# Kernel tuning notes

Hardware: AMD Instinct MI355X
Metric: run time of the kernel (lower is better)

## Reference

```python
import jax, jax.numpy as jnp
import numpy as np

B, S, TK, H, E, V, OOV = 16, 8, 400, 256, 128, 50000, 50
H2 = 2 * H


def setup_inputs() -> dict:
    key = jax.random.key(0)
    ks = jax.random.split(key, 24)
    std = 0.02
    d = {}
    d["y_t_1"] = jax.random.randint(ks[0], (B,), 0, V)
    d["h0"] = jax.random.normal(ks[1], (B, H), jnp.float32)
    d["c0"] = jax.random.normal(ks[2], (B, H), jnp.float32)
    d["encoder_output"] = jax.random.normal(ks[3], (B, S, TK, H2), jnp.float32)
    d["section_output"] = jax.random.normal(ks[4], (B, S, H2), jnp.float32)
    d["enc_padding_mask"] = jnp.ones((B, S, TK), jnp.float32)
    d["c_t_1"] = jax.random.normal(ks[5], (B, H2), jnp.float32)
    d["extra_zeros"] = jnp.zeros((B, OOV), jnp.float32)
    d["enc_batch_extend_vocab"] = jax.random.randint(ks[6], (B, S * TK), 0, V + OOV)
    d["coverage"] = jnp.zeros((B, S, TK), jnp.float32)
    d["gamma"] = jnp.ones((B, S, TK), jnp.float32)
    # learned parameters
    d["embedding"] = std * jax.random.normal(ks[7], (V, E), jnp.float32)
    d["W_xc"] = std * jax.random.normal(ks[8], (H2 + E, E), jnp.float32)
    d["b_xc"] = jnp.zeros((E,), jnp.float32)
    d["W_ih"] = std * jax.random.normal(ks[9], (E, 4 * H), jnp.float32)
    d["b_ih"] = jnp.zeros((4 * H,), jnp.float32)
    d["W_hh"] = std * jax.random.normal(ks[10], (H, 4 * H), jnp.float32)
    # pytorch init sets forget-gate bias (2nd quarter) to 1
    d["b_hh"] = jnp.zeros((4 * H,), jnp.float32).at[H:2 * H].set(1.0)
    d["Wh_sec"] = std * jax.random.normal(ks[11], (H2, H2), jnp.float32)
    d["Wd_sec"] = std * jax.random.normal(ks[12], (H2, H2), jnp.float32)
    d["bd_sec"] = jnp.zeros((H2,), jnp.float32)
    d["v_sec"] = std * jax.random.normal(ks[13], (H2, 1), jnp.float32)
    d["Wh_w"] = std * jax.random.normal(ks[14], (H2, H2), jnp.float32)
    d["Wc_w"] = std * jax.random.normal(ks[15], (H2,), jnp.float32)
    d["Wd_w"] = std * jax.random.normal(ks[16], (H2, H2), jnp.float32)
    d["bd_w"] = jnp.zeros((H2,), jnp.float32)
    d["v_w"] = std * jax.random.normal(ks[17], (H2, 1), jnp.float32)
    d["W_pgen"] = std * jax.random.normal(ks[18], (4 * H + E, 1), jnp.float32)
    d["b_pgen"] = jnp.zeros((1,), jnp.float32)
    d["W_out1"] = std * jax.random.normal(ks[19], (3 * H, H), jnp.float32)
    d["b_out1"] = jnp.zeros((H,), jnp.float32)
    d["W_out2"] = std * jax.random.normal(ks[20], (H, V), jnp.float32)
    d["b_out2"] = jnp.zeros((V,), jnp.float32)
    return d


def reference(y_t_1, h0, c0, encoder_output, section_output, enc_padding_mask,
              c_t_1, extra_zeros, enc_batch_extend_vocab, coverage, gamma,
              embedding, W_xc, b_xc, W_ih, b_ih, W_hh, b_hh,
              Wh_sec, Wd_sec, bd_sec, v_sec,
              Wh_w, Wc_w, Wd_w, bd_w, v_w,
              W_pgen, b_pgen, W_out1, b_out1, W_out2, b_out2):
    # embedding + input context projection
    emb = embedding[y_t_1]                                      # [B,E]
    x = jnp.concatenate([c_t_1, emb], axis=1) @ W_xc + b_xc     # [B,E]
    # single-step LSTM (pytorch gate order i,f,g,o)
    gates = x @ W_ih + b_ih + h0 @ W_hh + b_hh                  # [B,4H]
    i, f, g, o = jnp.split(gates, 4, axis=1)
    c = jax.nn.sigmoid(f) * c0 + jax.nn.sigmoid(i) * jnp.tanh(g)
    h = jax.nn.sigmoid(o) * jnp.tanh(c)
    s_t_hat = jnp.concatenate([h, c], axis=1)                   # [B,2H]
    # section attention -> beta [B,S]
    e_sec = jnp.tanh(section_output @ Wh_sec + (s_t_hat @ Wd_sec + bd_sec)[:, None, :])
    sc_sec = jnp.squeeze(e_sec @ v_sec, -1)                     # [B,S]
    beta = jax.nn.softmax(sc_sec, axis=1)
    beta = beta / beta.sum(axis=1, keepdims=True)
    # word attention with coverage feature
    att = encoder_output @ Wh_w + (s_t_hat @ Wd_w + bd_w)[:, None, None, :]
    att = att + coverage[..., None] * Wc_w                      # [B,S,TK,2H]
    sc_w = jnp.squeeze(jnp.tanh(att) @ v_w, -1)                 # [B,S,TK]
    ws = (beta[:, :, None] * sc_w).reshape(B, S * TK)
    mask = enc_padding_mask.reshape(B, S * TK)
    ad = jax.nn.softmax(ws, axis=1) * mask
    attn = ad / ad.sum(axis=1, keepdims=True)                   # [B,S*TK]
    c_t = jnp.einsum('bt,btn->bn', attn, encoder_output.reshape(B, S * TK, H2))
    cov = coverage + attn.reshape(B, S, TK)
    # pointer-gen gate
    p_gen = jax.nn.sigmoid(jnp.concatenate([c_t, s_t_hat, x], axis=1) @ W_pgen + b_pgen)  # [B,1]
    # output vocab distribution
    out = jnp.concatenate([h, c_t], axis=1) @ W_out1 + b_out1
    vocab_dist = jax.nn.softmax(out @ W_out2 + b_out2, axis=1)  # [B,V]
    vd = jnp.concatenate([p_gen * vocab_dist, extra_zeros], axis=1)  # [B,V+OOV]
    ad_ = (1.0 - p_gen) * attn
    rows = jnp.arange(B)[:, None]
    final_dist = vd.at[rows, enc_batch_extend_vocab].add(ad_)
    return (final_dist, h, c, c_t, attn, p_gen, cov)
```

## Files before the change

kernel.cpp:

```cpp
#include <hip/hip_runtime.h>
#include <math.h>

#define BB   16
#define SS   8
#define TKK  400
#define HH   256
#define EE   128
#define VV   50000
#define OOVV 50
#define HH2  512
#define STK  (SS*TKK)
#define VOO  (VV+OOVV)

#define OFF_X     0
#define OFF_ST    2048
#define OFF_SD    10240
#define OFF_WD    18432
#define OFF_SCSEC 26752
#define OFF_SCW   26880
#define OFF_CT    78080
#define OFF_OUT1  86272
#define OFF_PGEN  90368
#define OFF_PSUM  93520
#define OFF_BT    113040

#define O_FD   0
#define O_H    800800
#define O_C    804896
#define O_CT   808992
#define O_ATTN 817184
#define O_PGEN 868384
#define O_COV  868400

#define NLB 391
#define GEMM_NB 800

typedef __attribute__((ext_vector_type(8))) short bf16x8;
typedef __attribute__((ext_vector_type(4))) float f32x4;

__device__ __forceinline__ float sigm(float x){ return 1.0f/(1.0f+expf(-x)); }

__device__ __forceinline__ unsigned short f2b(float f){
  unsigned int u = __float_as_uint(f);
  unsigned int r = (u + 0x7fffu + ((u >> 16) & 1u)) >> 16;
  return (unsigned short)r;
}

__device__ __forceinline__ float tanhfast(float x){
  float cx = fminf(9.0f, fmaxf(-9.0f, x));
  float t = __expf(2.0f*cx);
  return (t - 1.0f) * __builtin_amdgcn_rcpf(t + 1.0f);
}

__device__ __forceinline__ float wave_sum(float v){
  #pragma unroll
  for(int o=32;o>0;o>>=1) v += __shfl_xor(v,o);
  return v;
}
__device__ __forceinline__ float wave_max(float v){
  #pragma unroll
  for(int o=32;o>0;o>>=1) v = fmaxf(v,__shfl_xor(v,o));
  return v;
}

__device__ __forceinline__ void glds16(const void* g, void* l){
  __builtin_amdgcn_global_load_lds((const __attribute__((address_space(1))) void*)g,
                                   (__attribute__((address_space(3))) void*)l, 16, 0, 0);
}

__device__ __forceinline__ bf16x8 cvt8(float4 a, float4 b){
  union{ bf16x8 v; unsigned short u[8]; } t;
  t.u[0]=f2b(a.x); t.u[1]=f2b(a.y); t.u[2]=f2b(a.z); t.u[3]=f2b(a.w);
  t.u[4]=f2b(b.x); t.u[5]=f2b(b.y); t.u[6]=f2b(b.z); t.u[7]=f2b(b.w);
  return t.v;
}

__global__ void k_pre(const float* __restrict__ Whw, unsigned short* __restrict__ Btg,
                      const int* __restrict__ y, const float* __restrict__ ct1,
                      const float* __restrict__ emb, const float* __restrict__ Wxc,
                      const float* __restrict__ bxc, float* __restrict__ ws){
  __shared__ float sm[10440];
  int bi = blockIdx.x, tid = threadIdx.x;
  if(bi < 64){
    int n0 = (bi & 7)*64, k0 = (bi >> 3)*64;
    int tx = tid & 63, ty = tid >> 6;
    #pragma unroll
    for(int it=0; it<16; it++){
      int kk = it*4 + ty;
      sm[kk*65 + tx] = Whw[(size_t)(k0+kk)*HH2 + n0 + tx];
    }
    __syncthreads();
    #pragma unroll
    for(int it=0; it<2; it++){
      int kgl = it*4 + ty;
      int kgG = (k0 >> 3) + kgl;
      int rnd = kgG >> 2, kg = kgG & 3;
      int col = n0 + tx;
      union{ bf16x8 v; unsigned short u[8]; } t;
      #pragma unroll
      for(int j=0;j<8;j++) t.u[j] = f2b(sm[(kgl*8+j)*65 + tx]);
      *(bf16x8*)&Btg[(size_t)rnd*16384 + (size_t)(col*4 + (kg ^ ((col>>1)&3)))*8] = t.v;
    }
  } else if(bi < 80){
    float* cat = sm;
    float* red = sm + 10240;
    for(int f=tid; f<BB*640; f+=256){
      int b = f/640, r = f - b*640;
      cat[f] = (r < HH2) ? ct1[b*HH2 + r] : emb[(size_t)y[b]*EE + (r-HH2)];
    }
    __syncthreads();
    int c = (bi-64)*8 + (tid & 7);
    int b = (tid >> 3) & 15;
    int kh = tid >> 7;
    float acc = 0.0f;
    const float* a = &cat[b*640];
    for(int k=kh*320; k<kh*320+320; k++) acc += a[k]*Wxc[k*EE + c];
    if(kh==1) red[b*8 + (tid&7)] = acc;
    __syncthreads();
    if(kh==0) ws[OFF_X + b*EE + c] = acc + red[b*8 + (tid&7)] + bxc[c];
  } else {
    for(int f=tid; f<BB*HH2; f+=256) ws[OFF_CT + f] = 0.0f;
  }
}

__global__ void k_lstm(const float* __restrict__ h0, const float* __restrict__ c0,
                       const float* __restrict__ Wih, const float* __restrict__ bih,
                       const float* __restrict__ Whh, const float* __restrict__ bhh,
                       float* __restrict__ ws, float* __restrict__ out){
  __shared__ float xh[4*384];
  __shared__ float red[3*64*4];
  int tid = threadIdx.x;
  int jc = (blockIdx.x & 15)*16, bc = (blockIdx.x >> 4)*4;
  for(int f=tid; f<4*384; f+=256){
    int bl = f/384, r = f - bl*384;
    xh[f] = (r < EE) ? ws[OFF_X + (bc+bl)*EE + r] : h0[(bc+bl)*HH + (r-EE)];
  }
  __syncthreads();
  int jl = tid & 15, bl = (tid >> 4) & 3, kq = tid >> 6;
  int j = jc + jl, b = bc + bl;
  float a0=0.f, a1=0.f, a2=0.f, a3=0.f;
  const float* a = &xh[bl*384];
  for(int k=kq*96; k<kq*96+96; k++){
    float v = a[k];
    const float* w = (k < EE) ? &Wih[k*4*HH + j] : &Whh[(k-EE)*4*HH + j];
    a0 += v*w[0]; a1 += v*w[HH]; a2 += v*w[2*HH]; a3 += v*w[3*HH];
  }
  if(kq){
    float* r = &red[((kq-1)*64 + bl*16 + jl)*4];
    r[0]=a0; r[1]=a1; r[2]=a2; r[3]=a3;
  }
  __syncthreads();
  if(kq==0){
    #pragma unroll
    for(int p=0;p<3;p++){
      const float* r = &red[(p*64 + bl*16 + jl)*4];
      a0+=r[0]; a1+=r[1]; a2+=r[2]; a3+=r[3];
    }
    a0 += bih[j] + bhh[j];
    a1 += bih[j+HH] + bhh[j+HH];
    a2 += bih[j+2*HH] + bhh[j+2*HH];
    a3 += bih[j+3*HH] + bhh[j+3*HH];
    float c = sigm(a1)*c0[b*HH+j] + sigm(a0)*tanhf(a2);
    float h = sigm(a3)*tanhf(c);
    out[O_H + b*HH + j] = h;
    out[O_C + b*HH + j] = c;
    ws[OFF_ST + b*HH2 + j]      = h;
    ws[OFF_ST + b*HH2 + HH + j] = c;
  }
}

__global__ void k_proj(const float* __restrict__ Wdsec, const float* __restrict__ bdsec,
                       const float* __restrict__ Wdw,  const float* __restrict__ bdw,
                       float* __restrict__ ws){
  __shared__ float st[BB*HH2];
  __shared__ float red[128];
  int tid = threadIdx.x;
  for(int f=tid; f<BB*HH2; f+=256) st[f] = ws[OFF_ST + f];
  __syncthreads();
  int mi = blockIdx.x >> 6;
  int c = (blockIdx.x & 63)*8 + (tid & 7);
  int bl = (tid >> 3) & 15;
  int kq = tid >> 7;
  const float* Wm = mi ? Wdw : Wdsec;
  const float* bias = mi ? bdw : bdsec;
  int dst = mi ? OFF_WD : OFF_SD;
  float acc = 0.0f;
  const float* a = &st[bl*HH2];
  for(int k=kq*256; k<kq*256+256; k++) acc += a[k]*Wm[k*HH2 + c];
  if(kq==1) red[bl*8 + (tid&7)] = acc;
  __syncthreads();
  if(kq==0) ws[dst + bl*HH2 + c] = acc + red[bl*8 + (tid&7)] + bias[c];
}

__global__ __launch_bounds__(512, 4) void k_gemm6(
        const float* __restrict__ A, const unsigned short* __restrict__ Btg,
        const float* __restrict__ Wcw, const float* __restrict__ vw,
        const float* __restrict__ cover,
        const float* __restrict__ sec, const float* __restrict__ Whsec,
        const float* __restrict__ vsec, float* __restrict__ ws){
  __shared__ __align__(16) unsigned short smem[32768];
  int tid = threadIdx.x;
  if(blockIdx.x >= GEMM_NB){
    float* row = (float*)smem;
    float* red = row + HH2;
    int bi = blockIdx.x - GEMM_NB;
    int b = bi >> 3;
    if(tid < HH2) row[tid] = sec[(size_t)bi*HH2 + tid];
    __syncthreads();
    int col = tid;
    float acc = 0.0f;
    #pragma unroll 8
    for(int k=0;k<HH2;k++) acc += row[k]*Whsec[k*HH2 + col];
    float val = tanhf(acc + ws[OFF_SD + b*HH2 + col]) * vsec[col];
    val = wave_sum(val);
    if((tid&63)==0) red[tid>>6] = val;
    __syncthreads();
    if(tid==0){
      float s = 0.0f;
      #pragma unroll
      for(int i=0;i<8;i++) s += red[i];
      ws[OFF_SCSEC + bi] = s;
    }
    return;
  }
  int w = tid >> 6, lane = tid & 63, m = lane & 15, q = lane >> 4;
  int mk = (m >> 1) & 3, sw = q ^ mk;
  int rg = w >> 1, cg = w & 1;
  int row0 = blockIdx.x * 64;
  int b = blockIdx.x / 50;

  const float* arow_p = &A[(size_t)(row0 + rg*16 + m)*HH2 + q*8];

  f32x4 acc[16];
  #pragma unroll
  for(int j=0;j<16;j++) acc[j] = (f32x4){0.f,0.f,0.f,0.f};

  #define GLDSB(rr, bufsel) {                                                  \
    const unsigned short* bsrc_ = Btg + (size_t)(rr)*16384;                    \
    _Pragma("unroll")                                                          \
    for(int i_=0;i_<4;i_++)                                                    \
      glds16(bsrc_ + i_*4096 + tid*8, &smem[(bufsel)*16384 + i_*4096 + tid*8]);\
  }

  GLDSB(0, 0);
  float4 pa0 = *(const float4*)(arow_p);
  float4 pa1 = *(const float4*)(arow_p + 4);
  GLDSB(1, 1);
  asm volatile("s_waitcnt vmcnt(6)" ::: "memory");
  __builtin_amdgcn_sched_barrier(0);
  bf16x8 af = cvt8(pa0, pa1);
  __builtin_amdgcn_s_barrier();

  #pragma unroll
  for(int r=0; r<16; r++){
    if(r < 15){
      pa0 = *(const float4*)(arow_p + (r+1)*32);
      pa1 = *(const float4*)(arow_p + (r+1)*32 + 4);
    }
    __builtin_amdgcn_s_setprio(1);
    #pragma unroll
    for(int cf=0; cf<16; cf++){
      int col = cg*256 + cf*16 + m;
      bf16x8 bv = *(const bf16x8*)&smem[(size_t)(r&1)*16384 + ((size_t)col*4 + sw)*8];
      acc[cf] = __builtin_amdgcn_mfma_f32_16x16x32_bf16(af, bv, acc[cf], 0,0,0);
    }
    __builtin_amdgcn_s_setprio(0);
    if(r < 14){
      asm volatile("s_waitcnt lgkmcnt(0)" ::: "memory");
      __builtin_amdgcn_sched_barrier(0);
      __builtin_amdgcn_s_barrier();
      GLDSB(r+2, (r&1));
    }
    if(r < 15){
      if(r < 14){ asm volatile("s_waitcnt vmcnt(6)" ::: "memory"); }
      else      { asm volatile("s_waitcnt vmcnt(2)" ::: "memory"); }
      __builtin_amdgcn_sched_barrier(0);
      af = cvt8(pa0, pa1);
      __builtin_amdgcn_s_barrier();
    }
  }
  #undef GLDSB

  float cov[4];
  #pragma unroll
  for(int r=0;r<4;r++) cov[r] = cover[row0 + rg*16 + q*4 + r];
  float rsum[4] = {0,0,0,0};
  #pragma unroll
  for(int j=0;j<16;j++){
    int col = cg*256 + j*16 + m;
    float wdv = ws[OFF_WD + b*HH2 + col];
    float wcv = Wcw[col], vwv = vw[col];
    #pragma unroll
    for(int r=0;r<4;r++)
      rsum[r] += tanhfast(acc[j][r] + wdv + cov[r]*wcv) * vwv;
  }
  __syncthreads();
  float* rbuf = (float*)smem;
  #pragma unroll
  for(int r=0;r<4;r++){
    float v = rsum[r];
    v += __shfl_xor(v,1,16); v += __shfl_xor(v,2,16);
    v += __shfl_xor(v,4,16); v += __shfl_xor(v,8,16);
    if(m==0) rbuf[cg*64 + rg*16 + q*4 + r] = v;
  }
  __syncthreads();
  if(tid < 64) ws[OFF_SCW + row0 + tid] = rbuf[tid] + rbuf[64 + tid];
}

__global__ void k_attn(const float* __restrict__ mask, const float* __restrict__ cover,
                       float* __restrict__ ws, float* __restrict__ out){
  int b = blockIdx.x, tid = threadIdx.x;
  __shared__ float vals[STK];
  __shared__ float red[4];
  __shared__ float sc[SS];
  if(tid < SS) sc[tid] = ws[OFF_SCSEC + b*SS + tid];
  __syncthreads();
  float bm = -1e30f;
  #pragma unroll
  for(int s=0;s<SS;s++) bm = fmaxf(bm, sc[s]);
  float be[SS]; float bsum = 0.0f;
  #pragma unroll
  for(int s=0;s<SS;s++){ be[s] = expf(sc[s]-bm); bsum += be[s]; }
  #pragma unroll
  for(int s=0;s<SS;s++) be[s] /= bsum;
  int lane = tid & 63, w = tid >> 6;
  float m = -1e30f;
  for(int j=tid;j<STK;j+=256){
    float v = be[j/TKK] * ws[OFF_SCW + b*STK + j];
    vals[j] = v; m = fmaxf(m, v);
  }
  m = wave_max(m);
  if(lane==0) red[w] = m;
  __syncthreads();
  m = fmaxf(fmaxf(red[0],red[1]), fmaxf(red[2],red[3]));
  __syncthreads();
  float ssum = 0.0f;
  for(int j=tid;j<STK;j+=256){
    float e = expf(vals[j]-m) * mask[b*STK + j];
    vals[j] = e; ssum += e;
  }
  ssum = wave_sum(ssum);
  if(lane==0) red[w] = ssum;
  __syncthreads();
  float inv = 1.0f/(red[0]+red[1]+red[2]+red[3]);
  for(int j=tid;j<STK;j+=256){
    float a = vals[j]*inv;
    out[O_ATTN + b*STK + j] = a;
    out[O_COV  + b*STK + j] = cover[b*STK + j] + a;
  }
}

__global__ void k_ct(const float* __restrict__ enc, const float* __restrict__ out,
                     float* __restrict__ ws){
  int b = blockIdx.y, tid = threadIdx.x;
  __shared__ float a[64];
  __shared__ float part[512];
  int t0 = blockIdx.x*64;
  if(tid<64) a[tid] = out[O_ATTN + b*STK + t0 + tid];
  __syncthreads();
  int c4 = tid & 127, rh = tid >> 7;
  const float4* e4 = (const float4*)enc;
  size_t base = ((size_t)(b*STK + t0 + rh*32))*128 + c4;
  float4 acc = {0.f,0.f,0.f,0.f};
  #pragma unroll 8
  for(int rr=0; rr<32; rr++){
    float4 v = e4[base + (size_t)rr*128];
    float av = a[rh*32 + rr];
    acc.x += av*v.x; acc.y += av*v.y; acc.z += av*v.z; acc.w += av*v.w;
  }
  if(rh) *(float4*)&part[c4*4] = acc;
  __syncthreads();
  if(!rh){
    float4 o = *(const float4*)&part[c4*4];
    atomicAdd(&ws[OFF_CT + b*HH2 + c4*4 + 0], acc.x + o.x);
    atomicAdd(&ws[OFF_CT + b*HH2 + c4*4 + 1], acc.y + o.y);
    atomicAdd(&ws[OFF_CT + b*HH2 + c4*4 + 2], acc.z + o.z);
    atomicAdd(&ws[OFF_CT + b*HH2 + c4*4 + 3], acc.w + o.w);
  }
}

__global__ void k_out1(const float* __restrict__ Wp, const float* __restrict__ bp,
                       const float* __restrict__ Wo1, const float* __restrict__ bo1,
                       float* __restrict__ ws, float* __restrict__ out){
  __shared__ float cat[BB*768];
  __shared__ float red[3*64];
  int tid = threadIdx.x;
  if(blockIdx.x == 64){
    int w = tid >> 6, lane = tid & 63;
    #pragma unroll
    for(int i=0;i<4;i++){
      int b = w*4 + i;
      float p = 0.0f;
      for(int k=lane;k<4*HH+EE;k+=64){
        float val = (k < HH2) ? ws[OFF_CT + b*HH2 + k]
                  : (k < 4*HH) ? ws[OFF_ST + b*HH2 + (k-HH2)]
                  : ws[OFF_X + b*EE + (k-4*HH)];
        p += val * Wp[k];
      }
      p = wave_sum(p);
      if(lane==0){
        float pg = sigm(p + bp[0]);
        ws[OFF_PGEN + b] = pg;
        out[O_PGEN + b]  = pg;
      }
    }
    for(int f=tid; f<BB*HH2; f+=256) out[O_CT + f] = ws[OFF_CT + f];
    return;
  }
  for(int f=tid; f<BB*768; f+=256){
    int b = f/768, r = f - b*768;
    cat[f] = (r < HH) ? ws[OFF_ST + b*HH2 + r] : ws[OFF_CT + b*HH2 + (r-HH)];
  }
  __syncthreads();
  int cl = tid & 3, bl = (tid >> 2) & 15, kq = tid >> 6;
  int c = blockIdx.x*4 + cl;
  float acc = 0.0f;
  const float* a = &cat[bl*768];
  for(int k=kq*192; k<kq*192+192; k++) acc += a[k]*Wo1[k*HH + c];
  if(kq) red[(kq-1)*64 + bl*4 + cl] = acc;
  __syncthreads();
  if(kq==0){
    acc += red[bl*4+cl] + red[64 + bl*4+cl] + red[128 + bl*4+cl];
    ws[OFF_OUT1 + bl*HH + c] = acc + bo1[c];
  }
}

__global__ void k_logits(const float* __restrict__ W2, const float* __restrict__ b2,
                         float* __restrict__ ws, float* __restrict__ out){
  int tid = threadIdx.x;
  __shared__ float o1[BB*HH];
  for(int i=tid;i<BB*HH/4;i+=256)
    ((float4*)o1)[i] = ((const float4*)&ws[OFF_OUT1])[i];
  __syncthreads();
  int cl = tid & 31, bq = tid >> 5;
  int c4 = blockIdx.x*128 + cl*4;
  bool ok = c4 < VV;
  int b0 = bq*2, b1 = b0+1;
  float4 acc0 = {0.f,0.f,0.f,0.f}, acc1 = {0.f,0.f,0.f,0.f};
  if(ok){
    const float* oa = &o1[b0*HH];
    const float* ob = &o1[b1*HH];
    #pragma unroll 4
    for(int k=0;k<HH;k++){
      float4 wv = *(const float4*)&W2[(size_t)k*VV + c4];
      float xa = oa[k], xb = ob[k];
      acc0.x += xa*wv.x; acc0.y += xa*wv.y; acc0.z += xa*wv.z; acc0.w += xa*wv.w;
      acc1.x += xb*wv.x; acc1.y += xb*wv.y; acc1.z += xb*wv.z; acc1.w += xb*wv.w;
    }
  }
  float bv[4] = {0,0,0,0};
  if(ok){ float4 t = *(const float4*)&b2[c4]; bv[0]=t.x; bv[1]=t.y; bv[2]=t.z; bv[3]=t.w; }
  float a0[4] = {acc0.x, acc0.y, acc0.z, acc0.w};
  float a1[4] = {acc1.x, acc1.y, acc1.z, acc1.w};
  float s0 = 0.0f, s1 = 0.0f;
  #pragma unroll
  for(int j=0;j<4;j++){
    float e0 = ok ? expf(a0[j]+bv[j]) : 0.0f;
    float e1 = ok ? expf(a1[j]+bv[j]) : 0.0f;
    if(ok){
      out[(size_t)b0*VOO + c4 + j] = e0;
      out[(size_t)b1*VOO + c4 + j] = e1;
    }
    s0 += e0; s1 += e1;
  }
  #pragma unroll
  for(int o=1;o<32;o<<=1){ s0 += __shfl_xor(s0,o,32); s1 += __shfl_xor(s1,o,32); }
  if(cl==0){
    ws[OFF_PSUM + b0*NLB + blockIdx.x] = s0;
    ws[OFF_PSUM + b1*NLB + blockIdx.x] = s1;
  }
}

__global__ void k_final(const float* __restrict__ xz, float* __restrict__ ws,
                        float* __restrict__ out){
  int b = blockIdx.y;
  int v = blockIdx.x*256 + threadIdx.x;
  __shared__ float red[4];
  int lane = threadIdx.x & 63, w = threadIdx.x >> 6;
  float p = 0.0f;
  for(int i=threadIdx.x;i<NLB;i+=256) p += ws[OFF_PSUM + b*NLB + i];
  p = wave_sum(p);
  if(lane==0) red[w] = p;
  __syncthreads();
  float s = red[0]+red[1]+red[2]+red[3];
  float pg = ws[OFF_PGEN + b];
  if(v < VV)       out[(size_t)b*VOO + v] = pg * out[(size_t)b*VOO + v] / s;
  else if(v < VOO) out[(size_t)b*VOO + v] = xz[b*OOVV + (v-VV)];
}

__global__ void k_scatter(const int* __restrict__ ebev, float* __restrict__ ws,
                          float* __restrict__ out){
  int b = blockIdx.x;
  float r = 1.0f - ws[OFF_PGEN + b];
  for(int j=threadIdx.x;j<STK;j+=256){
    int idx = ebev[b*STK + j];
    atomicAdd(&out[(size_t)b*VOO + idx], r*out[O_ATTN + b*STK + j]);
  }
}

extern "C" void kernel_launch(void* const* d_in, const int* in_sizes, int n_in,
                              void* d_out, int out_size, void* d_ws, size_t ws_size,
                              hipStream_t stream){
  const int*   y     = (const int*)  d_in[0];
  const float* h0    = (const float*)d_in[1];
  const float* c0    = (const float*)d_in[2];
  const float* enc   = (const float*)d_in[3];
  const float* sec   = (const float*)d_in[4];
  const float* mask  = (const float*)d_in[5];
  const float* ct1   = (const float*)d_in[6];
  const float* xz    = (const float*)d_in[7];
  const int*   ebev  = (const int*)  d_in[8];
  const float* cover = (const float*)d_in[9];
  const float* emb   = (const float*)d_in[11];
  const float* Wxc   = (const float*)d_in[12];
  const float* bxc   = (const float*)d_in[13];
  const float* Wih   = (const float*)d_in[14];
  const float* bih   = (const float*)d_in[15];
  const float* Whh   = (const float*)d_in[16];
  const float* bhh   = (const float*)d_in[17];
  const float* Whsec = (const float*)d_in[18];
  const float* Wdsec = (const float*)d_in[19];
  const float* bdsec = (const float*)d_in[20];
  const float* vsec  = (const float*)d_in[21];
  const float* Whw   = (const float*)d_in[22];
  const float* Wcw   = (const float*)d_in[23];
  const float* Wdw   = (const float*)d_in[24];
  const float* bdw   = (const float*)d_in[25];
  const float* vw    = (const float*)d_in[26];
  const float* Wp    = (const float*)d_in[27];
  const float* bp    = (const float*)d_in[28];
  const float* Wo1   = (const float*)d_in[29];
  const float* bo1   = (const float*)d_in[30];
  const float* Wo2   = (const float*)d_in[31];
  const float* bo2   = (const float*)d_in[32];
  float* out = (float*)d_out;
  float* ws  = (float*)d_ws;
  unsigned short* Btg = (unsigned short*)(ws + OFF_BT);

  k_pre    <<<dim3(81),       dim3(256), 0, stream>>>(Whw, Btg, y, ct1, emb, Wxc, bxc, ws);
  k_lstm   <<<dim3(64),       dim3(256), 0, stream>>>(h0, c0, Wih, bih, Whh, bhh, ws, out);
  k_proj   <<<dim3(128),      dim3(256), 0, stream>>>(Wdsec, bdsec, Wdw, bdw, ws);
  k_gemm6  <<<dim3(928),      dim3(512), 0, stream>>>(enc, Btg, Wcw, vw, cover, sec, Whsec, vsec, ws);
  k_attn   <<<dim3(BB),       dim3(256), 0, stream>>>(mask, cover, ws, out);
  k_ct     <<<dim3(50,BB),    dim3(256), 0, stream>>>(enc, out, ws);
  k_out1   <<<dim3(65),       dim3(256), 0, stream>>>(Wp, bp, Wo1, bo1, ws, out);
  k_logits <<<dim3(NLB),      dim3(256), 0, stream>>>(Wo2, bo2, ws, out);
  k_final  <<<dim3(196,BB),   dim3(256), 0, stream>>>(xz, ws, out);
  k_scatter<<<dim3(BB),       dim3(256), 0, stream>>>(ebev, ws, out);
}
```

Before: 487.6 us.

## Retile word-attention GEMM, split-K projection, widen attn and scatter kernels

The main GEMM changes its warp tiling from 4x2 to 2x4. Each wave now computes two 16-row A fragments against 8 column fragments, so every B fragment read from LDS is reused twice, and A loads are double-buffered two rounds ahead. The decoder projection becomes a split-K kernel with 64 blocks that accumulate via atomicAdd onto bias-initialised outputs, with the bias init moved into k_pre. The softmax kernel moves to 1024 threads and the scatter runs across 4x more blocks. Together these trade more register pressure and atomics for better LDS reuse and more parallelism in the small kernels.

```diff
diff --git a/kernel.cpp b/kernel.cpp
--- a/kernel.cpp
+++ b/kernel.cpp
@@ -78,7 +78,8 @@
 __global__ void k_pre(const float* __restrict__ Whw, unsigned short* __restrict__ Btg,
                       const int* __restrict__ y, const float* __restrict__ ct1,
                       const float* __restrict__ emb, const float* __restrict__ Wxc,
-                      const float* __restrict__ bxc, float* __restrict__ ws){
+                      const float* __restrict__ bxc, const float* __restrict__ bdsec,
+                      const float* __restrict__ bdw, float* __restrict__ ws){
   __shared__ float sm[10440];
   int bi = blockIdx.x, tid = threadIdx.x;
   if(bi < 64){
@@ -119,7 +120,12 @@
     __syncthreads();
     if(kh==0) ws[OFF_X + b*EE + c] = acc + red[b*8 + (tid&7)] + bxc[c];
   } else {
-    for(int f=tid; f<BB*HH2; f+=256) ws[OFF_CT + f] = 0.0f;
+    for(int f=tid; f<BB*HH2; f+=256){
+      int c = f & (HH2-1);
+      ws[OFF_CT + f] = 0.0f;
+      ws[OFF_SD + f] = bdsec[c];
+      ws[OFF_WD + f] = bdw[c];
+    }
   }
 }
 
@@ -169,27 +175,33 @@
   }
 }
 
-__global__ void k_proj(const float* __restrict__ Wdsec, const float* __restrict__ bdsec,
-                       const float* __restrict__ Wdw,  const float* __restrict__ bdw,
+__global__ void k_proj(const float* __restrict__ Wdsec, const float* __restrict__ Wdw,
                        float* __restrict__ ws){
-  __shared__ float st[BB*HH2];
-  __shared__ float red[128];
+  __shared__ float st[BB*32];
   int tid = threadIdx.x;
-  for(int f=tid; f<BB*HH2; f+=256) st[f] = ws[OFF_ST + f];
-  __syncthreads();
-  int mi = blockIdx.x >> 6;
-  int c = (blockIdx.x & 63)*8 + (tid & 7);
-  int bl = (tid >> 3) & 15;
-  int kq = tid >> 7;
-  const float* Wm = mi ? Wdw : Wdsec;
-  const float* bias = mi ? bdw : bdsec;
+  int mi = blockIdx.x >> 5;
+  int cb = (blockIdx.x >> 4) & 1;
+  int kq = blockIdx.x & 15;
+  int k0 = kq*32;
+  for(int f=tid; f<BB*32; f+=256){
+    int b = f >> 5, kk = f & 31;
+    st[f] = ws[OFF_ST + b*HH2 + k0 + kk];
+  }
+  __syncthreads();
+  int c = cb*256 + tid;
+  const float* Wm = (mi ? Wdw : Wdsec) + (size_t)k0*HH2 + c;
+  float acc[BB];
+  #pragma unroll
+  for(int b=0;b<BB;b++) acc[b] = 0.0f;
+  #pragma unroll 4
+  for(int kk=0;kk<32;kk++){
+    float wv = Wm[(size_t)kk*HH2];
+    #pragma unroll
+    for(int b=0;b<BB;b++) acc[b] += st[b*32 + kk]*wv;
+  }
   int dst = mi ? OFF_WD : OFF_SD;
-  float acc = 0.0f;
-  const float* a = &st[bl*HH2];
-  for(int k=kq*256; k<kq*256+256; k++) acc += a[k]*Wm[k*HH2 + c];
-  if(kq==1) red[bl*8 + (tid&7)] = acc;
-  __syncthreads();
-  if(kq==0) ws[dst + bl*HH2 + c] = acc + red[bl*8 + (tid&7)] + bias[c];
+  #pragma unroll
+  for(int b=0;b<BB;b++) atomicAdd(&ws[dst + b*HH2 + c], acc[b]);
 }
 
 __global__ __launch_bounds__(512, 4) void k_gemm6(
@@ -225,93 +237,115 @@
   }
   int w = tid >> 6, lane = tid & 63, m = lane & 15, q = lane >> 4;
   int mk = (m >> 1) & 3, sw = q ^ mk;
-  int rg = w >> 1, cg = w & 1;
+  int rg = w >> 2, cg = w & 3;
   int row0 = blockIdx.x * 64;
   int b = blockIdx.x / 50;
 
-  const float* arow_p = &A[(size_t)(row0 + rg*16 + m)*HH2 + q*8];
-
-  f32x4 acc[16];
-  #pragma unroll
-  for(int j=0;j<16;j++) acc[j] = (f32x4){0.f,0.f,0.f,0.f};
-
-  #define GLDSB(rr, bufsel) {                                                  \
+  const float* a0p = &A[(size_t)(row0 + rg*32 + m)*HH2 + q*8];
+  const float* a1p = a0p + (size_t)16*HH2;
+
+  f32x4 acc0[8], acc1[8];
+  #pragma unroll
+  for(int j=0;j<8;j++){ acc0[j] = (f32x4){0.f,0.f,0.f,0.f}; acc1[j] = (f32x4){0.f,0.f,0.f,0.f}; }
+
+  float4 pa[2][4];
+  bf16x8 af0, af1;
+
+  #define GLDSB(rr, buf) {                                                     \
     const unsigned short* bsrc_ = Btg + (size_t)(rr)*16384;                    \
+    unsigned short* ldst_ = &smem[(buf)*16384];                                \
     _Pragma("unroll")                                                          \
     for(int i_=0;i_<4;i_++)                                                    \
-      glds16(bsrc_ + i_*4096 + tid*8, &smem[(bufsel)*16384 + i_*4096 + tid*8]);\
+      glds16(bsrc_ + i_*4096 + tid*8, ldst_ + i_*4096 + tid*8);                \
+  }
+  #define LOADA(rr, s) {                                                       \
+    pa[s][0] = *(const float4*)(a0p + (rr)*32);                                \
+    pa[s][1] = *(const float4*)(a0p + (rr)*32 + 4);                            \
+    pa[s][2] = *(const float4*)(a1p + (rr)*32);                                \
+    pa[s][3] = *(const float4*)(a1p + (rr)*32 + 4);                            \
   }
 
   GLDSB(0, 0);
-  float4 pa0 = *(const float4*)(arow_p);
-  float4 pa1 = *(const float4*)(arow_p + 4);
+  LOADA(0, 0);
+  LOADA(1, 1);
   GLDSB(1, 1);
-  asm volatile("s_waitcnt vmcnt(6)" ::: "memory");
+  asm volatile("s_waitcnt vmcnt(8)" ::: "memory");
   __builtin_amdgcn_sched_barrier(0);
-  bf16x8 af = cvt8(pa0, pa1);
+  af0 = cvt8(pa[0][0], pa[0][1]);
+  af1 = cvt8(pa[0][2], pa[0][3]);
   __builtin_amdgcn_s_barrier();
 
   #pragma unroll
   for(int r=0; r<16; r++){
-    if(r < 15){
-      pa0 = *(const float4*)(arow_p + (r+1)*32);
-      pa1 = *(const float4*)(arow_p + (r+1)*32 + 4);
-    }
+    if(r <= 13) LOADA(r+2, r&1);
     __builtin_amdgcn_s_setprio(1);
     #pragma unroll
-    for(int cf=0; cf<16; cf++){
-      int col = cg*256 + cf*16 + m;
-      bf16x8 bv = *(const bf16x8*)&smem[(size_t)(r&1)*16384 + ((size_t)col*4 + sw)*8];
-      acc[cf] = __builtin_amdgcn_mfma_f32_16x16x32_bf16(af, bv, acc[cf], 0,0,0);
+    for(int cf=0; cf<8; cf++){
+      int col = cg*128 + cf*16 + m;
+      bf16x8 bv = *(const bf16x8*)&smem[(r&1)*16384 + ((size_t)col*4 + sw)*8];
+      acc0[cf] = __builtin_amdgcn_mfma_f32_16x16x32_bf16(af0, bv, acc0[cf], 0,0,0);
+      acc1[cf] = __builtin_amdgcn_mfma_f32_16x16x32_bf16(af1, bv, acc1[cf], 0,0,0);
     }
     __builtin_amdgcn_s_setprio(0);
-    if(r < 14){
+    if(r <= 13){
       asm volatile("s_waitcnt lgkmcnt(0)" ::: "memory");
       __builtin_amdgcn_sched_barrier(0);
       __builtin_amdgcn_s_barrier();
-      GLDSB(r+2, (r&1));
-    }
-    if(r < 15){
-      if(r < 14){ asm volatile("s_waitcnt vmcnt(6)" ::: "memory"); }
-      else      { asm volatile("s_waitcnt vmcnt(2)" ::: "memory"); }
+      GLDSB(r+2, r&1);
+    }
+    if(r <= 14){
+      if(r <= 13){ asm volatile("s_waitcnt vmcnt(8)" ::: "memory"); }
+      else       { asm volatile("s_waitcnt vmcnt(0)" ::: "memory"); }
       __builtin_amdgcn_sched_barrier(0);
-      af = cvt8(pa0, pa1);
+      af0 = cvt8(pa[(r+1)&1][0], pa[(r+1)&1][1]);
+      af1 = cvt8(pa[(r+1)&1][2], pa[(r+1)&1][3]);
       __builtin_amdgcn_s_barrier();
     }
   }
   #undef GLDSB
-
-  float cov[4];
-  #pragma unroll
-  for(int r=0;r<4;r++) cov[r] = cover[row0 + rg*16 + q*4 + r];
-  float rsum[4] = {0,0,0,0};
-  #pragma unroll
-  for(int j=0;j<16;j++){
-    int col = cg*256 + j*16 + m;
+  #undef LOADA
+
+  float cov0[4], cov1[4];
+  #pragma unroll
+  for(int r=0;r<4;r++){
+    cov0[r] = cover[row0 + rg*32 + q*4 + r];
+    cov1[r] = cover[row0 + rg*32 + 16 + q*4 + r];
+  }
+  float rs0[4] = {0,0,0,0}, rs1[4] = {0,0,0,0};
+  #pragma unroll
+  for(int j=0;j<8;j++){
+    int col = cg*128 + j*16 + m;
     float wdv = ws[OFF_WD + b*HH2 + col];
     float wcv = Wcw[col], vwv = vw[col];
     #pragma unroll
-    for(int r=0;r<4;r++)
-      rsum[r] += tanhfast(acc[j][r] + wdv + cov[r]*wcv) * vwv;
+    for(int r=0;r<4;r++){
+      rs0[r] += tanhfast(acc0[j][r] + wdv + cov0[r]*wcv) * vwv;
+      rs1[r] += tanhfast(acc1[j][r] + wdv + cov1[r]*wcv) * vwv;
+    }
   }
   __syncthreads();
   float* rbuf = (float*)smem;
   #pragma unroll
   for(int r=0;r<4;r++){
-    float v = rsum[r];
+    float v = rs0[r];
     v += __shfl_xor(v,1,16); v += __shfl_xor(v,2,16);
     v += __shfl_xor(v,4,16); v += __shfl_xor(v,8,16);
-    if(m==0) rbuf[cg*64 + rg*16 + q*4 + r] = v;
-  }
-  __syncthreads();
-  if(tid < 64) ws[OFF_SCW + row0 + tid] = rbuf[tid] + rbuf[64 + tid];
+    if(m==0) rbuf[cg*64 + rg*32 + q*4 + r] = v;
+    float u = rs1[r];
+    u += __shfl_xor(u,1,16); u += __shfl_xor(u,2,16);
+    u += __shfl_xor(u,4,16); u += __shfl_xor(u,8,16);
+    if(m==0) rbuf[cg*64 + rg*32 + 16 + q*4 + r] = u;
+  }
+  __syncthreads();
+  if(tid < 64)
+    ws[OFF_SCW + row0 + tid] = rbuf[tid] + rbuf[64+tid] + rbuf[128+tid] + rbuf[192+tid];
 }
 
 __global__ void k_attn(const float* __restrict__ mask, const float* __restrict__ cover,
                        float* __restrict__ ws, float* __restrict__ out){
   int b = blockIdx.x, tid = threadIdx.x;
   __shared__ float vals[STK];
-  __shared__ float red[4];
+  __shared__ float redm[16], reds[16];
   __shared__ float sc[SS];
   if(tid < SS) sc[tid] = ws[OFF_SCSEC + b*SS + tid];
   __syncthreads();
@@ -325,25 +359,38 @@
   for(int s=0;s<SS;s++) be[s] /= bsum;
   int lane = tid & 63, w = tid >> 6;
   float m = -1e30f;
-  for(int j=tid;j<STK;j+=256){
+  for(int j=tid;j<STK;j+=1024){
     float v = be[j/TKK] * ws[OFF_SCW + b*STK + j];
     vals[j] = v; m = fmaxf(m, v);
   }
   m = wave_max(m);
-  if(lane==0) red[w] = m;
-  __syncthreads();
-  m = fmaxf(fmaxf(red[0],red[1]), fmaxf(red[2],red[3]));
-  __syncthreads();
+  if(lane==0) redm[w] = m;
+  __syncthreads();
+  if(tid < 16){
+    float t = redm[tid];
+    #pragma unroll
+    for(int o=8;o>0;o>>=1) t = fmaxf(t, __shfl_xor(t,o,16));
+    if(tid==0) redm[0] = t;
+  }
+  __syncthreads();
+  m = redm[0];
   float ssum = 0.0f;
-  for(int j=tid;j<STK;j+=256){
+  for(int j=tid;j<STK;j+=1024){
     float e = expf(vals[j]-m) * mask[b*STK + j];
     vals[j] = e; ssum += e;
   }
   ssum = wave_sum(ssum);
-  if(lane==0) red[w] = ssum;
-  __syncthreads();
-  float inv = 1.0f/(red[0]+red[1]+red[2]+red[3]);
-  for(int j=tid;j<STK;j+=256){
+  if(lane==0) reds[w] = ssum;
+  __syncthreads();
+  if(tid < 16){
+    float t = reds[tid];
+    #pragma unroll
+    for(int o=8;o>0;o>>=1) t += __shfl_xor(t,o,16);
+    if(tid==0) reds[0] = t;
+  }
+  __syncthreads();
+  float inv = 1.0f/reds[0];
+  for(int j=tid;j<STK;j+=1024){
     float a = vals[j]*inv;
     out[O_ATTN + b*STK + j] = a;
     out[O_COV  + b*STK + j] = cover[b*STK + j] + a;
@@ -490,9 +537,9 @@
 
 __global__ void k_scatter(const int* __restrict__ ebev, float* __restrict__ ws,
                           float* __restrict__ out){
-  int b = blockIdx.x;
+  int b = blockIdx.y;
   float r = 1.0f - ws[OFF_PGEN + b];
-  for(int j=threadIdx.x;j<STK;j+=256){
+  for(int j=blockIdx.x*256+threadIdx.x;j<STK;j+=1024){
     int idx = ebev[b*STK + j];
     atomicAdd(&out[(size_t)b*VOO + idx], r*out[O_ATTN + b*STK + j]);
   }
@@ -537,14 +584,14 @@
   float* ws  = (float*)d_ws;
   unsigned short* Btg = (unsigned short*)(ws + OFF_BT);
 
-  k_pre    <<<dim3(81),       dim3(256), 0, stream>>>(Whw, Btg, y, ct1, emb, Wxc, bxc, ws);
-  k_lstm   <<<dim3(64),       dim3(256), 0, stream>>>(h0, c0, Wih, bih, Whh, bhh, ws, out);
-  k_proj   <<<dim3(128),      dim3(256), 0, stream>>>(Wdsec, bdsec, Wdw, bdw, ws);
-  k_gemm6  <<<dim3(928),      dim3(512), 0, stream>>>(enc, Btg, Wcw, vw, cover, sec, Whsec, vsec, ws);
-  k_attn   <<<dim3(BB),       dim3(256), 0, stream>>>(mask, cover, ws, out);
-  k_ct     <<<dim3(50,BB),    dim3(256), 0, stream>>>(enc, out, ws);
-  k_out1   <<<dim3(65),       dim3(256), 0, stream>>>(Wp, bp, Wo1, bo1, ws, out);
-  k_logits <<<dim3(NLB),      dim3(256), 0, stream>>>(Wo2, bo2, ws, out);
-  k_final  <<<dim3(196,BB),   dim3(256), 0, stream>>>(xz, ws, out);
-  k_scatter<<<dim3(BB),       dim3(256), 0, stream>>>(ebev, ws, out);
-}
+  k_pre    <<<dim3(81),       dim3(256),  0, stream>>>(Whw, Btg, y, ct1, emb, Wxc, bxc, bdsec, bdw, ws);
+  k_lstm   <<<dim3(64),       dim3(256),  0, stream>>>(h0, c0, Wih, bih, Whh, bhh, ws, out);
+  k_proj   <<<dim3(64),       dim3(256),  0, stream>>>(Wdsec, Wdw, ws);
+  k_gemm6  <<<dim3(928),      dim3(512),  0, stream>>>(enc, Btg, Wcw, vw, cover, sec, Whsec, vsec, ws);
+  k_attn   <<<dim3(BB),       dim3(1024), 0, stream>>>(mask, cover, ws, out);
+  k_ct     <<<dim3(50,BB),    dim3(256),  0, stream>>>(enc, out, ws);
+  k_out1   <<<dim3(65),       dim3(256),  0, stream>>>(Wp, bp, Wo1, bo1, ws, out);
+  k_logits <<<dim3(NLB),      dim3(256),  0, stream>>>(Wo2, bo2, ws, out);
+  k_final  <<<dim3(196,BB),   dim3(256),  0, stream>>>(xz, ws, out);
+  k_scatter<<<dim3(4,BB),     dim3(256),  0, stream>>>(ebev, ws, out);
+}
```

Result: slower. 530.3 us (+8.7%).
